# Optimization experiments

Hardware: AMD Instinct MI355X
Metric: run time of the kernel (lower is better)

## Reference

```python
import jax, jax.numpy as jnp
import numpy as np
from jax import lax


def setup_inputs() -> dict:
    key = jax.random.key(0)
    k1, k2 = jax.random.split(key)
    L, B, d = 2048, 16, 1024
    x = jax.random.normal(k1, (L, B, d), dtype=jnp.float32)
    val_range = (3.0 / d) ** 0.5
    weight = jax.random.uniform(k2, (d, 3 * d), dtype=jnp.float32,
                                minval=-val_range, maxval=val_range)
    bias = jnp.zeros((2 * d,), dtype=jnp.float32)
    c0 = jnp.zeros((B, d), dtype=jnp.float32)
    return {"x": x, "weight": weight, "bias": bias, "c0": c0}


def reference(x, weight, bias, c0):
    # x: [L, B, d]; weight: [d, 3d]; bias: [2d]; c0: [B, d]
    L, B, d = x.shape
    u = (x.reshape(-1, d) @ weight).reshape(L, B, d, 3)
    x_tilde = u[..., 0]                               # [L, B, d]
    forget = jax.nn.sigmoid(u[..., 1] + bias[:d])     # [L, B, d]
    reset = jax.nn.sigmoid(u[..., 2] + bias[d:])      # [L, B, d]
    # k == 3 case: x_prime is the raw input (highway connection)
    x_prime = x

    def step(c_prev, ft_xt):
        ft, xt = ft_xt
        c = (c_prev - xt) * ft + xt
        return c, c

    c_last, cs = lax.scan(step, c0, (forget, x_tilde))
    g = jnp.tanh(cs)  # activation_type == 1
    h = (g - x_prime) * reset + x_prime
    return h, c_last
```

## Files before the change

### kernel.cpp

```cpp
#include <hip/hip_runtime.h>

#define L_SEQ 2048
#define BATCH 16
#define DDIM  1024
#define MDIM  (L_SEQ * BATCH)
#define NDIM  (3 * DDIM)
#define KDIM  DDIM
#define CH    (BATCH * DDIM)
#define NSEG  32
#define SEGL  64

typedef __attribute__((ext_vector_type(8))) short short8;
typedef __attribute__((ext_vector_type(4))) float f32x4;

static __device__ __forceinline__ unsigned short f2bf(float f) {
  unsigned int u = __builtin_bit_cast(unsigned int, f);
  unsigned int lsb = (u >> 16) & 1u;
  u += 0x7fffu + lsb;
  return (unsigned short)(u >> 16);
}
static __device__ __forceinline__ float bf2f(unsigned short s) {
  unsigned int u = ((unsigned int)s) << 16;
  return __builtin_bit_cast(float, u);
}

static __device__ __forceinline__ void gll16(const void* g, void* l) {
  __builtin_amdgcn_global_load_lds(
      (const __attribute__((address_space(1))) unsigned int*)g,
      (__attribute__((address_space(3))) unsigned int*)l, 16, 0, 0);
}


__global__ void k_convert_x(const float4* __restrict__ x, ushort4* __restrict__ xb, int n4) {
  int i = blockIdx.x * blockDim.x + threadIdx.x;
  int stride = gridDim.x * blockDim.x;
  for (; i < n4; i += stride) {
    float4 v = x[i];
    ushort4 o;
    o.x = f2bf(v.x); o.y = f2bf(v.y); o.z = f2bf(v.z); o.w = f2bf(v.w);
    xb[i] = o;
  }
}

__global__ void k_convert_w(const float* __restrict__ w, unsigned short* __restrict__ wb) {
  int gid = blockIdx.x * 256 + threadIdx.x;
  int k = gid & (KDIM - 1);
  int n = gid >> 10;
  int col = (n < DDIM) ? 3 * n : (n < 2 * DDIM) ? 3 * (n - DDIM) + 1 : 3 * (n - 2 * DDIM) + 2;
  wb[gid] = f2bf(w[(size_t)k * NDIM + col]);
}


#define MFMA16(QM)                                                             \
  acc[(QM)*4+0][0] = __builtin_amdgcn_mfma_f32_16x16x32_bf16(a0, b0, acc[(QM)*4+0][0], 0, 0, 0); \
  acc[(QM)*4+0][1] = __builtin_amdgcn_mfma_f32_16x16x32_bf16(a0, b1, acc[(QM)*4+0][1], 0, 0, 0); \
  acc[(QM)*4+0][2] = __builtin_amdgcn_mfma_f32_16x16x32_bf16(a0, b2, acc[(QM)*4+0][2], 0, 0, 0); \
  acc[(QM)*4+0][3] = __builtin_amdgcn_mfma_f32_16x16x32_bf16(a0, b3, acc[(QM)*4+0][3], 0, 0, 0); \
  acc[(QM)*4+1][0] = __builtin_amdgcn_mfma_f32_16x16x32_bf16(a1, b0, acc[(QM)*4+1][0], 0, 0, 0); \
  acc[(QM)*4+1][1] = __builtin_amdgcn_mfma_f32_16x16x32_bf16(a1, b1, acc[(QM)*4+1][1], 0, 0, 0); \
  acc[(QM)*4+1][2] = __builtin_amdgcn_mfma_f32_16x16x32_bf16(a1, b2, acc[(QM)*4+1][2], 0, 0, 0); \
  acc[(QM)*4+1][3] = __builtin_amdgcn_mfma_f32_16x16x32_bf16(a1, b3, acc[(QM)*4+1][3], 0, 0, 0); \
  acc[(QM)*4+2][0] = __builtin_amdgcn_mfma_f32_16x16x32_bf16(a2, b0, acc[(QM)*4+2][0], 0, 0, 0); \
  acc[(QM)*4+2][1] = __builtin_amdgcn_mfma_f32_16x16x32_bf16(a2, b1, acc[(QM)*4+2][1], 0, 0, 0); \
  acc[(QM)*4+2][2] = __builtin_amdgcn_mfma_f32_16x16x32_bf16(a2, b2, acc[(QM)*4+2][2], 0, 0, 0); \
  acc[(QM)*4+2][3] = __builtin_amdgcn_mfma_f32_16x16x32_bf16(a2, b3, acc[(QM)*4+2][3], 0, 0, 0); \
  acc[(QM)*4+3][0] = __builtin_amdgcn_mfma_f32_16x16x32_bf16(a3, b0, acc[(QM)*4+3][0], 0, 0, 0); \
  acc[(QM)*4+3][1] = __builtin_amdgcn_mfma_f32_16x16x32_bf16(a3, b1, acc[(QM)*4+3][1], 0, 0, 0); \
  acc[(QM)*4+3][2] = __builtin_amdgcn_mfma_f32_16x16x32_bf16(a3, b2, acc[(QM)*4+3][2], 0, 0, 0); \
  acc[(QM)*4+3][3] = __builtin_amdgcn_mfma_f32_16x16x32_bf16(a3, b3, acc[(QM)*4+3][3], 0, 0, 0);

#define BARRIER_FENCE() do {                    \
  __builtin_amdgcn_sched_barrier(0);            \
  __builtin_amdgcn_s_barrier();                 \
  asm volatile("" ::: "memory");                \
  __builtin_amdgcn_sched_barrier(0);            \
} while (0)

__global__ __launch_bounds__(512, 2) void k_gemm256(
    const unsigned short* __restrict__ xb,
    const unsigned short* __restrict__ wb,
    const float* __restrict__ bias,
    unsigned short* __restrict__ xtb,
    unsigned short* __restrict__ fbuf,
    unsigned short* __restrict__ rbuf) {
  __shared__ char LDS[131072];

  const int tid  = threadIdx.x;
  const int lane = tid & 63;
  const int wid  = tid >> 6;
  const int wr   = wid >> 2;
  const int wc   = wid & 3;

  int bid = blockIdx.x;
  int wg = (bid & 7) * 192 + (bid >> 3);
  int mt = wg / 12;
  int nt = wg - mt * 12;
  const int rowBase = mt * 256;
  const int colBase = nt * 256;

  const int l15 = lane & 15;
  const int sl  = lane >> 4;
  const int ra0 = wr * 128 + l15;
  const int rb0 = wc * 64 + l15;
  const int aRd = ra0 * 64 + (sl ^ ((ra0 >> 1) & 3)) * 16;
  const int bRd = rb0 * 64 + (sl ^ ((rb0 >> 1) & 3)) * 16;

  const int p0 = tid, p1 = 512 + tid;
  const int r0 = p0 >> 2, r1 = p1 >> 2;
  const int s0 = (p0 & 3) ^ ((r0 >> 1) & 3);
  const int s1 = (p1 & 3) ^ ((r1 >> 1) & 3);
  const char* srcA0 = (const char*)xb + (size_t)(rowBase + r0) * 2048 + s0 * 16;
  const char* srcA1 = (const char*)xb + (size_t)(rowBase + r1) * 2048 + s1 * 16;
  const char* srcB0 = (const char*)wb + (size_t)(colBase + r0) * 2048 + s0 * 16;
  const char* srcB1 = (const char*)wb + (size_t)(colBase + r1) * 2048 + s1 * 16;

  f32x4 acc[8][4];
#pragma unroll
  for (int i = 0; i < 8; ++i)
#pragma unroll
    for (int j = 0; j < 4; ++j)
      acc[i][j] = (f32x4){0.f, 0.f, 0.f, 0.f};

#pragma unroll
  for (int u = 0; u < 2; ++u) {
    char* ldsu = LDS + u * 32768;
    gll16(srcA0 + (size_t)u * 64, ldsu + wid * 1024);
    gll16(srcA1 + (size_t)u * 64, ldsu + 8192 + wid * 1024);
    gll16(srcB0 + (size_t)u * 64, ldsu + 16384 + wid * 1024);
    gll16(srcB1 + (size_t)u * 64, ldsu + 24576 + wid * 1024);
  }
  asm volatile("s_waitcnt vmcnt(4)" ::: "memory");
  __builtin_amdgcn_s_barrier();
  __builtin_amdgcn_sched_barrier(0);

#pragma unroll 4
  for (int t = 0; t < 32; ++t) {
    const int bi = t & 3;
    const int u = (t + 2) & 31;
    char* Ab = LDS + bi * 32768;
    char* Bb = Ab + 16384;
    char* ldsu = LDS + ((t + 2) & 3) * 32768;

    short8 a0 = *(const short8*)(Ab + aRd);
    short8 a1 = *(const short8*)(Ab + aRd + 1024);
    short8 a2 = *(const short8*)(Ab + aRd + 2048);
    short8 a3 = *(const short8*)(Ab + aRd + 3072);
    short8 b0 = *(const short8*)(Bb + bRd);
    short8 b1 = *(const short8*)(Bb + bRd + 1024);
    short8 b2 = *(const short8*)(Bb + bRd + 2048);
    short8 b3 = *(const short8*)(Bb + bRd + 3072);
    gll16(srcA0 + (size_t)u * 64, ldsu + wid * 1024);
    gll16(srcA1 + (size_t)u * 64, ldsu + 8192 + wid * 1024);
    BARRIER_FENCE();
    __builtin_amdgcn_s_setprio(1);
    MFMA16(0)
    __builtin_amdgcn_s_setprio(0);
    BARRIER_FENCE();

    a0 = *(const short8*)(Ab + aRd + 4096);
    a1 = *(const short8*)(Ab + aRd + 5120);
    a2 = *(const short8*)(Ab + aRd + 6144);
    a3 = *(const short8*)(Ab + aRd + 7168);
    gll16(srcB0 + (size_t)u * 64, ldsu + 16384 + wid * 1024);
    gll16(srcB1 + (size_t)u * 64, ldsu + 24576 + wid * 1024);
    BARRIER_FENCE();
    __builtin_amdgcn_s_setprio(1);
    MFMA16(1)
    __builtin_amdgcn_s_setprio(0);
    __builtin_amdgcn_sched_barrier(0);
    asm volatile("s_waitcnt vmcnt(4)" ::: "memory");
    BARRIER_FENCE();
  }

  const int region = colBase >> 10;
#pragma unroll
  for (int qm = 0; qm < 2; ++qm) {
#pragma unroll
    for (int m = 0; m < 4; ++m) {
      int grow = rowBase + wr * 128 + qm * 64 + m * 16 + ((lane >> 4) << 2);
#pragma unroll
      for (int n = 0; n < 4; ++n) {
        int gcol = colBase + wc * 64 + n * 16 + (lane & 15);
        f32x4 v = acc[qm * 4 + m][n];
        if (region == 0) {
#pragma unroll
          for (int j = 0; j < 4; ++j)
            xtb[(size_t)(grow + j) * DDIM + gcol] = f2bf(v[j]);
        } else {
          float bv = bias[gcol - DDIM];
          unsigned short* dst = (region == 1) ? fbuf : rbuf;
          int lcol = gcol - (region << 10);
#pragma unroll
          for (int j = 0; j < 4; ++j) {
            float sg = 1.0f / (1.0f + __expf(-(v[j] + bv)));
            dst[(size_t)(grow + j) * DDIM + lcol] = f2bf(sg);
          }
        }
      }
    }
  }
}


__global__ __launch_bounds__(256) void k_scan1(
    const unsigned short* __restrict__ fbuf,
    const unsigned short* __restrict__ xtb,
    float4* __restrict__ AB) {
  int chp = blockIdx.x * 256 + threadIdx.x;
  int seg = blockIdx.y;
  size_t base = (size_t)seg * SEGL * CH + chp * 2;
  const unsigned int* fp = (const unsigned int*)(fbuf + base);
  const unsigned int* xp = (const unsigned int*)(xtb + base);
  float a0 = 1.f, a1 = 1.f, b0 = 0.f, b1 = 0.f;
#pragma unroll 8
  for (int s = 0; s < SEGL; ++s) {
    unsigned int fv = fp[(size_t)s * (CH / 2)];
    unsigned int xv = xp[(size_t)s * (CH / 2)];
    float f0 = bf2f((unsigned short)fv), f1 = bf2f((unsigned short)(fv >> 16));
    float x0 = bf2f((unsigned short)xv), x1 = bf2f((unsigned short)(xv >> 16));
    b0 = (b0 - x0) * f0 + x0;  a0 *= f0;
    b1 = (b1 - x1) * f1 + x1;  a1 *= f1;
  }
  AB[(size_t)seg * (CH / 2) + chp] = (float4){a0, b0, a1, b1};
}


__global__ __launch_bounds__(256) void k_scan2(
    const float* __restrict__ c0,
    const float4* __restrict__ AB,
    float* __restrict__ Cin,
    float* __restrict__ clast) {
  int chp = blockIdx.x * 256 + threadIdx.x;
  float2 cc = ((const float2*)c0)[chp];
  float ca = cc.x, cb = cc.y;
#pragma unroll
  for (int s = 0; s < NSEG; ++s) {
    ((float2*)Cin)[(size_t)s * (CH / 2) + chp] = (float2){ca, cb};
    float4 ab = AB[(size_t)s * (CH / 2) + chp];
    ca = ca * ab.x + ab.y;
    cb = cb * ab.z + ab.w;
  }
  ((float2*)clast)[chp] = (float2){ca, cb};
}


__global__ __launch_bounds__(256) void k_scan3(
    const float* __restrict__ x,
    const unsigned short* __restrict__ fbuf,
    const unsigned short* __restrict__ xtb,
    const unsigned short* __restrict__ rbuf,
    const float* __restrict__ Cin,
    float* __restrict__ h) {
  int chp = blockIdx.x * 256 + threadIdx.x;
  int seg = blockIdx.y;
  float2 cc = ((const float2*)Cin)[(size_t)seg * (CH / 2) + chp];
  float ca = cc.x, cb = cc.y;
  size_t base = (size_t)seg * SEGL * CH + chp * 2;
  const unsigned int* fp = (const unsigned int*)(fbuf + base);
  const unsigned int* tp = (const unsigned int*)(xtb + base);
  const unsigned int* rp = (const unsigned int*)(rbuf + base);
  const float2* xp = (const float2*)(x + base);
  float2* hp = (float2*)(h + base);
#pragma unroll 4
  for (int s = 0; s < SEGL; ++s) {
    unsigned int fv = fp[(size_t)s * (CH / 2)];
    unsigned int tv = tp[(size_t)s * (CH / 2)];
    unsigned int rv = rp[(size_t)s * (CH / 2)];
    float2 xv = xp[(size_t)s * (CH / 2)];
    float f0 = bf2f((unsigned short)fv), f1 = bf2f((unsigned short)(fv >> 16));
    float t0 = bf2f((unsigned short)tv), t1 = bf2f((unsigned short)(tv >> 16));
    float r0 = bf2f((unsigned short)rv), r1 = bf2f((unsigned short)(rv >> 16));
    ca = (ca - t0) * f0 + t0;
    cb = (cb - t1) * f1 + t1;
    float e0 = __expf(-2.f * fabsf(ca));
    float e1 = __expf(-2.f * fabsf(cb));
    float g0 = copysignf((1.f - e0) / (1.f + e0), ca);
    float g1 = copysignf((1.f - e1) / (1.f + e1), cb);
    float h0 = (g0 - xv.x) * r0 + xv.x;
    float h1 = (g1 - xv.y) * r1 + xv.y;
    hp[(size_t)s * (CH / 2)] = (float2){h0, h1};
  }
}


extern "C" void kernel_launch(void* const* d_in, const int* in_sizes, int n_in,
                              void* d_out, int out_size, void* d_ws, size_t ws_size,
                              hipStream_t stream) {
  const float* x    = (const float*)d_in[0];
  const float* w    = (const float*)d_in[1];
  const float* bias = (const float*)d_in[2];
  const float* c0   = (const float*)d_in[3];
  float* out = (float*)d_out;
  char* ws = (char*)d_ws;

  unsigned short* wb   = (unsigned short*)(ws);
  float4*         AB   = (float4*)(ws);
  float*          Cin  = (float*)(ws + 4194304);
  unsigned short* xtb  = (unsigned short*)(ws + 6291456);
  unsigned short* fbuf = (unsigned short*)(ws + 73400320);
  unsigned short* rbuf = (unsigned short*)(ws + 140509184);
  unsigned short* xb = (unsigned short*)d_out;

  k_convert_x<<<2048, 256, 0, stream>>>((const float4*)x, (ushort4*)xb, MDIM * KDIM / 4);
  k_convert_w<<<(NDIM * KDIM) / 256, 256, 0, stream>>>(w, wb);

  k_gemm256<<<1536, 512, 0, stream>>>(xb, wb, bias, xtb, fbuf, rbuf);

  k_scan1<<<dim3(32, NSEG), 256, 0, stream>>>(fbuf, xtb, AB);
  k_scan2<<<32, 256, 0, stream>>>(c0, AB, Cin, out + (size_t)L_SEQ * CH);
  k_scan3<<<dim3(32, NSEG), 256, 0, stream>>>(x, fbuf, xtb, rbuf, Cin, out);
}
```

Baseline: 411.0 us.

## Software-pipeline LDS fragment loads across K tiles with one barrier per tile

Restructures the GEMM main loop so the A and B fragments for the next K tile are read from LDS while the current tile's second MFMA half runs. B fragments are double-buffered in registers (even/odd sets). The four barriers per iteration become one, which is meant to cut synchronisation stalls and hide LDS latency behind MFMA work. This raises register pressure, and the reduced barrier count could open race windows on the 4-stage LDS ring if the ordering is wrong.

```diff
diff --git a/kernel.cpp b/kernel.cpp
--- a/kernel.cpp
+++ b/kernel.cpp
@@ -51,29 +51,50 @@
 }
 
 
-#define MFMA16(QM)                                                             \
-  acc[(QM)*4+0][0] = __builtin_amdgcn_mfma_f32_16x16x32_bf16(a0, b0, acc[(QM)*4+0][0], 0, 0, 0); \
-  acc[(QM)*4+0][1] = __builtin_amdgcn_mfma_f32_16x16x32_bf16(a0, b1, acc[(QM)*4+0][1], 0, 0, 0); \
-  acc[(QM)*4+0][2] = __builtin_amdgcn_mfma_f32_16x16x32_bf16(a0, b2, acc[(QM)*4+0][2], 0, 0, 0); \
-  acc[(QM)*4+0][3] = __builtin_amdgcn_mfma_f32_16x16x32_bf16(a0, b3, acc[(QM)*4+0][3], 0, 0, 0); \
-  acc[(QM)*4+1][0] = __builtin_amdgcn_mfma_f32_16x16x32_bf16(a1, b0, acc[(QM)*4+1][0], 0, 0, 0); \
-  acc[(QM)*4+1][1] = __builtin_amdgcn_mfma_f32_16x16x32_bf16(a1, b1, acc[(QM)*4+1][1], 0, 0, 0); \
-  acc[(QM)*4+1][2] = __builtin_amdgcn_mfma_f32_16x16x32_bf16(a1, b2, acc[(QM)*4+1][2], 0, 0, 0); \
-  acc[(QM)*4+1][3] = __builtin_amdgcn_mfma_f32_16x16x32_bf16(a1, b3, acc[(QM)*4+1][3], 0, 0, 0); \
-  acc[(QM)*4+2][0] = __builtin_amdgcn_mfma_f32_16x16x32_bf16(a2, b0, acc[(QM)*4+2][0], 0, 0, 0); \
-  acc[(QM)*4+2][1] = __builtin_amdgcn_mfma_f32_16x16x32_bf16(a2, b1, acc[(QM)*4+2][1], 0, 0, 0); \
-  acc[(QM)*4+2][2] = __builtin_amdgcn_mfma_f32_16x16x32_bf16(a2, b2, acc[(QM)*4+2][2], 0, 0, 0); \
-  acc[(QM)*4+2][3] = __builtin_amdgcn_mfma_f32_16x16x32_bf16(a2, b3, acc[(QM)*4+2][3], 0, 0, 0); \
-  acc[(QM)*4+3][0] = __builtin_amdgcn_mfma_f32_16x16x32_bf16(a3, b0, acc[(QM)*4+3][0], 0, 0, 0); \
-  acc[(QM)*4+3][1] = __builtin_amdgcn_mfma_f32_16x16x32_bf16(a3, b1, acc[(QM)*4+3][1], 0, 0, 0); \
-  acc[(QM)*4+3][2] = __builtin_amdgcn_mfma_f32_16x16x32_bf16(a3, b2, acc[(QM)*4+3][2], 0, 0, 0); \
-  acc[(QM)*4+3][3] = __builtin_amdgcn_mfma_f32_16x16x32_bf16(a3, b3, acc[(QM)*4+3][3], 0, 0, 0);
-
-#define BARRIER_FENCE() do {                    \
-  __builtin_amdgcn_sched_barrier(0);            \
-  __builtin_amdgcn_s_barrier();                 \
-  asm volatile("" ::: "memory");                \
-  __builtin_amdgcn_sched_barrier(0);            \
+#define MFMA1(I, J, A, B) \
+  acc[I][J] = __builtin_amdgcn_mfma_f32_16x16x32_bf16(A, B, acc[I][J], 0, 0, 0);
+
+#define MFMAQ(BASE, A0, A1, A2, A3, B0, B1, B2, B3)  \
+  MFMA1(BASE + 0, 0, A0, B0) MFMA1(BASE + 0, 1, A0, B1) \
+  MFMA1(BASE + 0, 2, A0, B2) MFMA1(BASE + 0, 3, A0, B3) \
+  MFMA1(BASE + 1, 0, A1, B0) MFMA1(BASE + 1, 1, A1, B1) \
+  MFMA1(BASE + 1, 2, A1, B2) MFMA1(BASE + 1, 3, A1, B3) \
+  MFMA1(BASE + 2, 0, A2, B0) MFMA1(BASE + 2, 1, A2, B1) \
+  MFMA1(BASE + 2, 2, A2, B2) MFMA1(BASE + 2, 3, A2, B3) \
+  MFMA1(BASE + 3, 0, A3, B0) MFMA1(BASE + 3, 1, A3, B1) \
+  MFMA1(BASE + 3, 2, A3, B2) MFMA1(BASE + 3, 3, A3, B3)
+
+#define TILE(J, X0, X1, X2, X3, Y0, Y1, Y2, Y3) do {                         \
+  const char* Ab  = LDSc + (((J)) & 3) * 32768;                              \
+  const char* AbN = LDSc + (((J) + 1) & 3) * 32768;                          \
+  char* Sb = LDSc + (((J) + 2) & 3) * 32768;                                 \
+  const int kbS = ((i * 4 + (J) + 2) & 31) * 64;                             \
+  q0 = *(const short8*)(Ab + aRd + 4096);                                    \
+  q1 = *(const short8*)(Ab + aRd + 5120);                                    \
+  q2 = *(const short8*)(Ab + aRd + 6144);                                    \
+  q3 = *(const short8*)(Ab + aRd + 7168);                                    \
+  gll16(srcA0 + kbS, Sb + dstOff);                                           \
+  gll16(srcA1 + kbS, Sb + 8192 + dstOff);                                    \
+  __builtin_amdgcn_s_setprio(1);                                             \
+  MFMAQ(0, p0, p1, p2, p3, X0, X1, X2, X3)                                   \
+  __builtin_amdgcn_s_setprio(0);                                             \
+  gll16(srcB0 + kbS, Sb + 16384 + dstOff);                                   \
+  gll16(srcB1 + kbS, Sb + 24576 + dstOff);                                   \
+  __builtin_amdgcn_sched_barrier(0);                                         \
+  asm volatile("s_waitcnt vmcnt(4)" ::: "memory");                           \
+  __builtin_amdgcn_s_barrier();                                              \
+  __builtin_amdgcn_sched_barrier(0);                                         \
+  p0 = *(const short8*)(AbN + aRd);                                          \
+  p1 = *(const short8*)(AbN + aRd + 1024);                                   \
+  p2 = *(const short8*)(AbN + aRd + 2048);                                   \
+  p3 = *(const short8*)(AbN + aRd + 3072);                                   \
+  Y0 = *(const short8*)(AbN + 16384 + bRd);                                  \
+  Y1 = *(const short8*)(AbN + 16384 + bRd + 1024);                           \
+  Y2 = *(const short8*)(AbN + 16384 + bRd + 2048);                           \
+  Y3 = *(const short8*)(AbN + 16384 + bRd + 3072);                           \
+  __builtin_amdgcn_s_setprio(1);                                             \
+  MFMAQ(4, q0, q1, q2, q3, X0, X1, X2, X3)                                   \
+  __builtin_amdgcn_s_setprio(0);                                             \
 } while (0)
 
 __global__ __launch_bounds__(512, 2) void k_gemm256(
@@ -84,6 +105,7 @@
     unsigned short* __restrict__ fbuf,
     unsigned short* __restrict__ rbuf) {
   __shared__ char LDS[131072];
+  char* LDSc = LDS;
 
   const int tid  = threadIdx.x;
   const int lane = tid & 63;
@@ -105,72 +127,56 @@
   const int aRd = ra0 * 64 + (sl ^ ((ra0 >> 1) & 3)) * 16;
   const int bRd = rb0 * 64 + (sl ^ ((rb0 >> 1) & 3)) * 16;
 
-  const int p0 = tid, p1 = 512 + tid;
-  const int r0 = p0 >> 2, r1 = p1 >> 2;
-  const int s0 = (p0 & 3) ^ ((r0 >> 1) & 3);
-  const int s1 = (p1 & 3) ^ ((r1 >> 1) & 3);
+  const int p0i = tid, p1i = 512 + tid;
+  const int r0 = p0i >> 2, r1 = p1i >> 2;
+  const int s0 = (p0i & 3) ^ ((r0 >> 1) & 3);
+  const int s1 = (p1i & 3) ^ ((r1 >> 1) & 3);
   const char* srcA0 = (const char*)xb + (size_t)(rowBase + r0) * 2048 + s0 * 16;
   const char* srcA1 = (const char*)xb + (size_t)(rowBase + r1) * 2048 + s1 * 16;
   const char* srcB0 = (const char*)wb + (size_t)(colBase + r0) * 2048 + s0 * 16;
   const char* srcB1 = (const char*)wb + (size_t)(colBase + r1) * 2048 + s1 * 16;
+  const int dstOff = wid * 1024;
 
   f32x4 acc[8][4];
 #pragma unroll
-  for (int i = 0; i < 8; ++i)
-#pragma unroll
-    for (int j = 0; j < 4; ++j)
-      acc[i][j] = (f32x4){0.f, 0.f, 0.f, 0.f};
+  for (int ii = 0; ii < 8; ++ii)
+#pragma unroll
+    for (int jj = 0; jj < 4; ++jj)
+      acc[ii][jj] = (f32x4){0.f, 0.f, 0.f, 0.f};
 
 #pragma unroll
   for (int u = 0; u < 2; ++u) {
-    char* ldsu = LDS + u * 32768;
-    gll16(srcA0 + (size_t)u * 64, ldsu + wid * 1024);
-    gll16(srcA1 + (size_t)u * 64, ldsu + 8192 + wid * 1024);
-    gll16(srcB0 + (size_t)u * 64, ldsu + 16384 + wid * 1024);
-    gll16(srcB1 + (size_t)u * 64, ldsu + 24576 + wid * 1024);
+    char* ldsu = LDSc + u * 32768;
+    gll16(srcA0 + u * 64, ldsu + dstOff);
+    gll16(srcA1 + u * 64, ldsu + 8192 + dstOff);
+    gll16(srcB0 + u * 64, ldsu + 16384 + dstOff);
+    gll16(srcB1 + u * 64, ldsu + 24576 + dstOff);
   }
   asm volatile("s_waitcnt vmcnt(4)" ::: "memory");
   __builtin_amdgcn_s_barrier();
   __builtin_amdgcn_sched_barrier(0);
 
-#pragma unroll 4
-  for (int t = 0; t < 32; ++t) {
-    const int bi = t & 3;
-    const int u = (t + 2) & 31;
-    char* Ab = LDS + bi * 32768;
-    char* Bb = Ab + 16384;
-    char* ldsu = LDS + ((t + 2) & 3) * 32768;
-
-    short8 a0 = *(const short8*)(Ab + aRd);
-    short8 a1 = *(const short8*)(Ab + aRd + 1024);
-    short8 a2 = *(const short8*)(Ab + aRd + 2048);
-    short8 a3 = *(const short8*)(Ab + aRd + 3072);
-    short8 b0 = *(const short8*)(Bb + bRd);
-    short8 b1 = *(const short8*)(Bb + bRd + 1024);
-    short8 b2 = *(const short8*)(Bb + bRd + 2048);
-    short8 b3 = *(const short8*)(Bb + bRd + 3072);
-    gll16(srcA0 + (size_t)u * 64, ldsu + wid * 1024);
-    gll16(srcA1 + (size_t)u * 64, ldsu + 8192 + wid * 1024);
-    BARRIER_FENCE();
-    __builtin_amdgcn_s_setprio(1);
-    MFMA16(0)
-    __builtin_amdgcn_s_setprio(0);
-    BARRIER_FENCE();
-
-    a0 = *(const short8*)(Ab + aRd + 4096);
-    a1 = *(const short8*)(Ab + aRd + 5120);
-    a2 = *(const short8*)(Ab + aRd + 6144);
-    a3 = *(const short8*)(Ab + aRd + 7168);
-    gll16(srcB0 + (size_t)u * 64, ldsu + 16384 + wid * 1024);
-    gll16(srcB1 + (size_t)u * 64, ldsu + 24576 + wid * 1024);
-    BARRIER_FENCE();
-    __builtin_amdgcn_s_setprio(1);
-    MFMA16(1)
-    __builtin_amdgcn_s_setprio(0);
-    __builtin_amdgcn_sched_barrier(0);
-    asm volatile("s_waitcnt vmcnt(4)" ::: "memory");
-    BARRIER_FENCE();
-  }
+  short8 p0, p1, p2, p3;
+  short8 q0, q1, q2, q3;
+  short8 e0, e1, e2, e3;
+  short8 o0, o1, o2, o3;
+
+  p0 = *(const short8*)(LDSc + aRd);
+  p1 = *(const short8*)(LDSc + aRd + 1024);
+  p2 = *(const short8*)(LDSc + aRd + 2048);
+  p3 = *(const short8*)(LDSc + aRd + 3072);
+  e0 = *(const short8*)(LDSc + 16384 + bRd);
+  e1 = *(const short8*)(LDSc + 16384 + bRd + 1024);
+  e2 = *(const short8*)(LDSc + 16384 + bRd + 2048);
+  e3 = *(const short8*)(LDSc + 16384 + bRd + 3072);
+
+  for (int i = 0; i < 8; ++i) {
+    TILE(0, e0, e1, e2, e3, o0, o1, o2, o3);
+    TILE(1, o0, o1, o2, o3, e0, e1, e2, e3);
+    TILE(2, e0, e1, e2, e3, o0, o1, o2, o3);
+    TILE(3, o0, o1, o2, o3, e0, e1, e2, e3);
+  }
+  asm volatile("s_waitcnt vmcnt(0)" ::: "memory");
 
   const int region = colBase >> 10;
 #pragma unroll
```

After: 409.3 us (median of 3 runs). About the same (-0.4%).
